# Kernel optimization log

Measured on AMD Instinct MI355X. Metric: run time of the kernel, lower is better.

## Reference

```python
import jax, jax.numpy as jnp
import numpy as np

HIDDEN = 128
STATE = 256
SEQ = 4096
BATCH = 16


def _op(q_i, q_j):
    # Binary operator for the parallel scan of the 2x2 block-diagonal recurrence.
    # m: (..., 4, N) holding [A, B, C, D] blocks; f: (..., 2, N) holding [b1, b2].
    m_i, f_i = q_i
    m_j, f_j = q_j
    iA, iB, iC, iD = m_i[..., 0, :], m_i[..., 1, :], m_i[..., 2, :], m_i[..., 3, :]
    jA, jB, jC, jD = m_j[..., 0, :], m_j[..., 1, :], m_j[..., 2, :], m_j[..., 3, :]
    m_new = jnp.stack([
        jA * iA + jB * iC,
        jA * iB + jB * iD,
        jC * iA + jD * iC,
        jC * iB + jD * iD,
    ], axis=-2)
    b1, b2 = f_i[..., 0, :], f_i[..., 1, :]
    f_new = jnp.stack([jA * b1 + jB * b2, jC * b1 + jD * b2], axis=-2) + f_j
    return m_new, f_new


def _apply_linoss_im(A_diag, B, x, step):
    # x: (L, H); B: (N, H); A_diag, step: (N,)
    Bu = x @ B.T                                    # (L, N)
    s2A = step ** 2 * A_diag
    schur = 1.0 / (1.0 + s2A)
    M11 = 1.0 - s2A * schur
    M12 = -step * A_diag * schur
    M21 = step * schur
    M22 = schur
    L, N = x.shape[0], A_diag.shape[0]
    M = jnp.broadcast_to(jnp.stack([M11, M12, M21, M22]), (L, 4, N))  # (L, 4, N)
    F = jnp.stack([M11 * Bu * step, M21 * Bu * step], axis=1)          # (L, 2, N)
    _, xs = jax.lax.associative_scan(_op, (M, F))
    return xs[:, 1, :]  # second state component y_k, shape (L, N)


def setup_inputs() -> dict:
    key = jax.random.key(0)
    kx, kA, ks, kB, kC, kD = jax.random.split(key, 6)
    x = jax.random.normal(kx, (BATCH, SEQ, HIDDEN), dtype=jnp.float32)
    A_diag = jax.random.uniform(kA, (STATE,), dtype=jnp.float32)
    steps = 0.5 * jax.random.normal(ks, (STATE,), dtype=jnp.float32)
    B = jax.random.normal(kB, (STATE, HIDDEN), dtype=jnp.float32) / np.sqrt(HIDDEN)
    C = jax.random.normal(kC, (HIDDEN, STATE), dtype=jnp.float32) / np.sqrt(STATE)
    D = jax.random.normal(kD, (HIDDEN,), dtype=jnp.float32)
    return {"x": x, "A_diag": A_diag, "steps": steps, "B": B, "C": C, "D": D}


def reference(x, A_diag, steps, B, C, D):
    # Parameter projections used by the mixer (LinOSS-IM, non-damped):
    step = jax.nn.sigmoid(steps)
    A = jax.nn.relu(A_diag)

    def per_seq(xs):
        ys = _apply_linoss_im(A, B, xs, step)   # (L, N)
        return ys @ C.T + D * xs                # (L, H)

    return jax.vmap(per_seq)(x)  # (B, L, H)
```

## Files before the change

kernel.cpp:

```cpp
#include <hip/hip_runtime.h>
#include <hip/hip_bf16.h>

#define BATCHN 16
#define SEQ 4096
#define HIDDEN 128
#define STATE 256
#define MTOT (BATCHN*SEQ)
#define NCHUNK 64
#define LCHUNK 64

typedef __bf16 bf16;
typedef __bf16 bf16x4 __attribute__((ext_vector_type(4)));
typedef __bf16 bf16x8 __attribute__((ext_vector_type(8)));
typedef float f32x4 __attribute__((ext_vector_type(4)));

__global__ __launch_bounds__(256) void setup_k(const float* __restrict__ A_diag,
        const float* __restrict__ steps, const float* __restrict__ Bm,
        const float* __restrict__ Cm, bf16* __restrict__ Bbf, bf16* __restrict__ Cbf,
        float* __restrict__ prm) {
    int idx = blockIdx.x * 256 + threadIdx.x;
    if (idx < STATE * HIDDEN) {
        Bbf[idx] = (bf16)Bm[idx];
        Cbf[idx] = (bf16)Cm[idx];
    }
    if (blockIdx.x == 0) {
        int n = threadIdx.x;
        float st = 1.0f / (1.0f + expf(-steps[n]));
        float A  = fmaxf(A_diag[n], 0.0f);
        float s2A = st * st * A;
        float schur = 1.0f / (1.0f + s2A);
        float m11 = 1.0f - s2A * schur;
        float m12 = -st * A * schur;
        float m21 = st * schur;
        float m22 = schur;
        prm[0*STATE+n] = m11;
        prm[1*STATE+n] = m12;
        prm[2*STATE+n] = m21;
        prm[3*STATE+n] = m22;
        prm[4*STATE+n] = m11 * st;
        prm[5*STATE+n] = m21 * st;
    }
}

__global__ __launch_bounds__(256) void gemm_xB(const float* __restrict__ x,
        const bf16* __restrict__ Bbf, bf16* __restrict__ Bu) {
    __shared__ bf16 lds[64][136];
    const int tid = threadIdx.x;
    const int m0 = blockIdx.x * 64;
    #pragma unroll
    for (int p = 0; p < 8; ++p) {
        int flat = p * 256 + tid;
        int row = flat >> 5;
        int c4  = flat & 31;
        float4 v = *reinterpret_cast<const float4*>(&x[(size_t)(m0 + row) * HIDDEN + c4 * 4]);
        bf16x4 w = { (bf16)v.x, (bf16)v.y, (bf16)v.z, (bf16)v.w };
        *reinterpret_cast<bf16x4*>(&lds[row][c4 * 4]) = w;
    }
    __syncthreads();
    const int wid = tid >> 6, lane = tid & 63;
    const int lr = lane & 15;
    const int lk = (lane >> 4) * 8;
    const int n0 = wid * 64;
    f32x4 acc[4][4];
    #pragma unroll
    for (int i = 0; i < 4; ++i)
        #pragma unroll
        for (int j = 0; j < 4; ++j) acc[i][j] = f32x4{0.f, 0.f, 0.f, 0.f};
    #pragma unroll
    for (int ks = 0; ks < 4; ++ks) {
        int k = ks * 32 + lk;
        bf16x8 a[4], b[4];
        #pragma unroll
        for (int mf = 0; mf < 4; ++mf)
            a[mf] = *reinterpret_cast<const bf16x8*>(&lds[mf * 16 + lr][k]);
        #pragma unroll
        for (int nf = 0; nf < 4; ++nf)
            b[nf] = *reinterpret_cast<const bf16x8*>(&Bbf[(size_t)(n0 + nf * 16 + lr) * HIDDEN + k]);
        #pragma unroll
        for (int mf = 0; mf < 4; ++mf)
            #pragma unroll
            for (int nf = 0; nf < 4; ++nf)
                acc[mf][nf] = __builtin_amdgcn_mfma_f32_16x16x32_bf16(a[mf], b[nf], acc[mf][nf], 0, 0, 0);
    }
    const int mrow = (lane >> 4) * 4;
    #pragma unroll
    for (int mf = 0; mf < 4; ++mf)
        #pragma unroll
        for (int nf = 0; nf < 4; ++nf)
            #pragma unroll
            for (int r = 0; r < 4; ++r) {
                int m = m0 + mf * 16 + mrow + r;
                int n = n0 + nf * 16 + lr;
                Bu[(size_t)m * STATE + n] = (bf16)acc[mf][nf][r];
            }
}

__global__ __launch_bounds__(256) void scan_part(const bf16* __restrict__ Bu,
        const float* __restrict__ prm, float* __restrict__ cs) {
    const int n = threadIdx.x;
    const int chunk = blockIdx.x & (NCHUNK - 1);
    const int b = blockIdx.x >> 6;
    const float m11 = prm[n], m12 = prm[STATE + n], m21 = prm[2*STATE + n],
                m22 = prm[3*STATE + n], c1 = prm[4*STATE + n], c2 = prm[5*STATE + n];
    float s1 = 0.f, s2 = 0.f;
    const bf16* p = &Bu[((size_t)(b * SEQ) + chunk * LCHUNK) * STATE + n];
    #pragma unroll 8
    for (int i = 0; i < LCHUNK; ++i) {
        float bu = (float)p[(size_t)i * STATE];
        float ns1 = fmaf(m11, s1, fmaf(m12, s2, c1 * bu));
        float ns2 = fmaf(m21, s1, fmaf(m22, s2, c2 * bu));
        s1 = ns1; s2 = ns2;
    }
    size_t base = ((size_t)(b * NCHUNK + chunk) * 2) * STATE + n;
    cs[base] = s1;
    cs[base + STATE] = s2;
}

__global__ __launch_bounds__(256) void scan_comb(float* __restrict__ cs,
        const float* __restrict__ prm) {
    const int n = threadIdx.x;
    const int b = blockIdx.x;
    float p11 = prm[n], p12 = prm[STATE + n], p21 = prm[2*STATE + n], p22 = prm[3*STATE + n];
    #pragma unroll
    for (int i = 0; i < 6; ++i) {
        float q11 = p11 * p11 + p12 * p21;
        float q12 = p11 * p12 + p12 * p22;
        float q21 = p21 * p11 + p22 * p21;
        float q22 = p21 * p12 + p22 * p22;
        p11 = q11; p12 = q12; p21 = q21; p22 = q22;
    }
    float S1 = 0.f, S2 = 0.f;
    #pragma unroll 8
    for (int c = 0; c < NCHUNK; ++c) {
        size_t base = ((size_t)(b * NCHUNK + c) * 2) * STATE + n;
        float q1 = cs[base], q2 = cs[base + STATE];
        cs[base] = S1; cs[base + STATE] = S2;
        float n1 = fmaf(p11, S1, fmaf(p12, S2, q1));
        float n2 = fmaf(p21, S1, fmaf(p22, S2, q2));
        S1 = n1; S2 = n2;
    }
}

__global__ __launch_bounds__(256) void scan_final(bf16* __restrict__ Bu,
        const float* __restrict__ prm, const float* __restrict__ cs) {
    const int n = threadIdx.x;
    const int chunk = blockIdx.x & (NCHUNK - 1);
    const int b = blockIdx.x >> 6;
    const float m11 = prm[n], m12 = prm[STATE + n], m21 = prm[2*STATE + n],
                m22 = prm[3*STATE + n], c1 = prm[4*STATE + n], c2 = prm[5*STATE + n];
    size_t cbase = ((size_t)(b * NCHUNK + chunk) * 2) * STATE + n;
    float s1 = cs[cbase], s2 = cs[cbase + STATE];
    bf16* p = &Bu[((size_t)(b * SEQ) + chunk * LCHUNK) * STATE + n];
    #pragma unroll 8
    for (int i = 0; i < LCHUNK; ++i) {
        float bu = (float)p[(size_t)i * STATE];
        float ns1 = fmaf(m11, s1, fmaf(m12, s2, c1 * bu));
        float ns2 = fmaf(m21, s1, fmaf(m22, s2, c2 * bu));
        s1 = ns1; s2 = ns2;
        p[(size_t)i * STATE] = (bf16)s2;
    }
}

__global__ __launch_bounds__(256) void gemm_yC(const bf16* __restrict__ y,
        const bf16* __restrict__ Cbf, const float* __restrict__ x,
        const float* __restrict__ Dv, float* __restrict__ out) {
    __shared__ bf16 lds[64][264];
    const int tid = threadIdx.x;
    const int m0 = blockIdx.x * 64;
    #pragma unroll
    for (int p = 0; p < 8; ++p) {
        int flat = p * 256 + tid;
        int row = flat >> 5;
        int c8  = flat & 31;
        bf16x8 v = *reinterpret_cast<const bf16x8*>(&y[(size_t)(m0 + row) * STATE + c8 * 8]);
        *reinterpret_cast<bf16x8*>(&lds[row][c8 * 8]) = v;
    }
    __syncthreads();
    const int wid = tid >> 6, lane = tid & 63;
    const int lr = lane & 15;
    const int lk = (lane >> 4) * 8;
    const int h0 = wid * 32;
    f32x4 acc[4][2];
    #pragma unroll
    for (int i = 0; i < 4; ++i) {
        acc[i][0] = f32x4{0.f, 0.f, 0.f, 0.f};
        acc[i][1] = f32x4{0.f, 0.f, 0.f, 0.f};
    }
    #pragma unroll
    for (int ks = 0; ks < 8; ++ks) {
        int k = ks * 32 + lk;
        bf16x8 a[4], bb[2];
        #pragma unroll
        for (int mf = 0; mf < 4; ++mf)
            a[mf] = *reinterpret_cast<const bf16x8*>(&lds[mf * 16 + lr][k]);
        #pragma unroll
        for (int hf = 0; hf < 2; ++hf)
            bb[hf] = *reinterpret_cast<const bf16x8*>(&Cbf[(size_t)(h0 + hf * 16 + lr) * STATE + k]);
        #pragma unroll
        for (int mf = 0; mf < 4; ++mf)
            #pragma unroll
            for (int hf = 0; hf < 2; ++hf)
                acc[mf][hf] = __builtin_amdgcn_mfma_f32_16x16x32_bf16(a[mf], bb[hf], acc[mf][hf], 0, 0, 0);
    }
    const int mrow = (lane >> 4) * 4;
    #pragma unroll
    for (int mf = 0; mf < 4; ++mf)
        #pragma unroll
        for (int hf = 0; hf < 2; ++hf) {
            int h = h0 + hf * 16 + lr;
            float d = Dv[h];
            #pragma unroll
            for (int r = 0; r < 4; ++r) {
                int m = m0 + mf * 16 + mrow + r;
                out[(size_t)m * HIDDEN + h] = acc[mf][hf][r] + d * x[(size_t)m * HIDDEN + h];
            }
        }
}

extern "C" void kernel_launch(void* const* d_in, const int* in_sizes, int n_in,
                              void* d_out, int out_size, void* d_ws, size_t ws_size,
                              hipStream_t stream) {
    const float* x      = (const float*)d_in[0];
    const float* A_diag = (const float*)d_in[1];
    const float* steps  = (const float*)d_in[2];
    const float* Bm     = (const float*)d_in[3];
    const float* Cm     = (const float*)d_in[4];
    const float* Dv     = (const float*)d_in[5];
    float* out = (float*)d_out;

    char* ws = (char*)d_ws;
    const size_t BU_BYTES = (size_t)MTOT * STATE * 2;
    const size_t CS_BYTES = (size_t)BATCHN * NCHUNK * 2 * STATE * 4;
    bf16*  Bu  = (bf16*)ws;
    float* cs  = (float*)(ws + BU_BYTES);
    bf16*  Bbf = (bf16*)(ws + BU_BYTES + CS_BYTES);
    bf16*  Cbf = (bf16*)(ws + BU_BYTES + CS_BYTES + (size_t)STATE * HIDDEN * 2);
    float* prm = (float*)(ws + BU_BYTES + CS_BYTES + (size_t)STATE * HIDDEN * 4);

    hipLaunchKernelGGL(setup_k, dim3(128), dim3(256), 0, stream, A_diag, steps, Bm, Cm, Bbf, Cbf, prm);
    hipLaunchKernelGGL(gemm_xB, dim3(MTOT / 64), dim3(256), 0, stream, x, Bbf, Bu);
    hipLaunchKernelGGL(scan_part, dim3(BATCHN * NCHUNK), dim3(256), 0, stream, Bu, prm, cs);
    hipLaunchKernelGGL(scan_comb, dim3(BATCHN), dim3(256), 0, stream, cs, prm);
    hipLaunchKernelGGL(scan_final, dim3(BATCHN * NCHUNK), dim3(256), 0, stream, Bu, prm, cs);
    hipLaunchKernelGGL(gemm_yC, dim3(MTOT / 64), dim3(256), 0, stream, Bu, Cbf, x, Dv, out);
}
```

Baseline: 69.04 us.

## Fuse GEMMs with chunked scan in LDS, recomputing x@B instead of storing Bu

Replaces the five-kernel pipeline with two fused kernels. The first computes the x@B tile into LDS and runs the intra-chunk scan to emit chunk carries. The second recomputes the same tile, applies the carried-in scan and the C projection entirely in LDS, and takes the skip term from the bf16 LDS copy of x. This removes the 32 MB bf16 Bu round trips through global memory and two launches, at the cost of doing the first GEMM twice and using more LDS per block. The skip term now uses bf16-rounded x, which slightly lowers its precision.

```diff
diff --git a/kernel.cpp b/kernel.cpp
--- a/kernel.cpp
+++ b/kernel.cpp
@@ -42,11 +42,8 @@
     }
 }
 
-__global__ __launch_bounds__(256) void gemm_xB(const float* __restrict__ x,
-        const bf16* __restrict__ Bbf, bf16* __restrict__ Bu) {
-    __shared__ bf16 lds[64][136];
-    const int tid = threadIdx.x;
-    const int m0 = blockIdx.x * 64;
+__device__ __forceinline__ void stage_x(const float* __restrict__ x, int m0, int tid,
+                                        bf16 (*xl)[136]) {
     #pragma unroll
     for (int p = 0; p < 8; ++p) {
         int flat = p * 256 + tid;
@@ -54,9 +51,12 @@
         int c4  = flat & 31;
         float4 v = *reinterpret_cast<const float4*>(&x[(size_t)(m0 + row) * HIDDEN + c4 * 4]);
         bf16x4 w = { (bf16)v.x, (bf16)v.y, (bf16)v.z, (bf16)v.w };
-        *reinterpret_cast<bf16x4*>(&lds[row][c4 * 4]) = w;
-    }
-    __syncthreads();
+        *reinterpret_cast<bf16x4*>(&xl[row][c4 * 4]) = w;
+    }
+}
+
+__device__ __forceinline__ void gemm1_to_lds(const bf16 (*xl)[136],
+        const bf16* __restrict__ Bbf, int tid, bf16 (*bu)[264]) {
     const int wid = tid >> 6, lane = tid & 63;
     const int lr = lane & 15;
     const int lk = (lane >> 4) * 8;
@@ -72,7 +72,7 @@
         bf16x8 a[4], b[4];
         #pragma unroll
         for (int mf = 0; mf < 4; ++mf)
-            a[mf] = *reinterpret_cast<const bf16x8*>(&lds[mf * 16 + lr][k]);
+            a[mf] = *reinterpret_cast<const bf16x8*>(&xl[mf * 16 + lr][k]);
         #pragma unroll
         for (int nf = 0; nf < 4; ++nf)
             b[nf] = *reinterpret_cast<const bf16x8*>(&Bbf[(size_t)(n0 + nf * 16 + lr) * HIDDEN + k]);
@@ -88,29 +88,34 @@
         #pragma unroll
         for (int nf = 0; nf < 4; ++nf)
             #pragma unroll
-            for (int r = 0; r < 4; ++r) {
-                int m = m0 + mf * 16 + mrow + r;
-                int n = n0 + nf * 16 + lr;
-                Bu[(size_t)m * STATE + n] = (bf16)acc[mf][nf][r];
-            }
-}
-
-__global__ __launch_bounds__(256) void scan_part(const bf16* __restrict__ Bu,
-        const float* __restrict__ prm, float* __restrict__ cs) {
-    const int n = threadIdx.x;
-    const int chunk = blockIdx.x & (NCHUNK - 1);
-    const int b = blockIdx.x >> 6;
+            for (int r = 0; r < 4; ++r)
+                bu[mf * 16 + mrow + r][n0 + nf * 16 + lr] = (bf16)acc[mf][nf][r];
+}
+
+__global__ __launch_bounds__(256) void k1_gemm_scanA(const float* __restrict__ x,
+        const bf16* __restrict__ Bbf, const float* __restrict__ prm,
+        float* __restrict__ cs) {
+    __shared__ bf16 xl[64][136];
+    __shared__ bf16 bu[64][264];
+    const int tid = threadIdx.x;
+    const int m0 = blockIdx.x * 64;
+    stage_x(x, m0, tid, xl);
+    __syncthreads();
+    gemm1_to_lds(xl, Bbf, tid, bu);
+    __syncthreads();
+    const int n = tid;
     const float m11 = prm[n], m12 = prm[STATE + n], m21 = prm[2*STATE + n],
                 m22 = prm[3*STATE + n], c1 = prm[4*STATE + n], c2 = prm[5*STATE + n];
     float s1 = 0.f, s2 = 0.f;
-    const bf16* p = &Bu[((size_t)(b * SEQ) + chunk * LCHUNK) * STATE + n];
     #pragma unroll 8
-    for (int i = 0; i < LCHUNK; ++i) {
-        float bu = (float)p[(size_t)i * STATE];
-        float ns1 = fmaf(m11, s1, fmaf(m12, s2, c1 * bu));
-        float ns2 = fmaf(m21, s1, fmaf(m22, s2, c2 * bu));
+    for (int t = 0; t < LCHUNK; ++t) {
+        float v = (float)bu[t][n];
+        float ns1 = fmaf(m11, s1, fmaf(m12, s2, c1 * v));
+        float ns2 = fmaf(m21, s1, fmaf(m22, s2, c2 * v));
         s1 = ns1; s2 = ns2;
     }
+    const int b = m0 >> 12;
+    const int chunk = (m0 >> 6) & (NCHUNK - 1);
     size_t base = ((size_t)(b * NCHUNK + chunk) * 2) * STATE + n;
     cs[base] = s1;
     cs[base + STATE] = s2;
@@ -141,50 +146,45 @@
     }
 }
 
-__global__ __launch_bounds__(256) void scan_final(bf16* __restrict__ Bu,
-        const float* __restrict__ prm, const float* __restrict__ cs) {
-    const int n = threadIdx.x;
-    const int chunk = blockIdx.x & (NCHUNK - 1);
-    const int b = blockIdx.x >> 6;
-    const float m11 = prm[n], m12 = prm[STATE + n], m21 = prm[2*STATE + n],
-                m22 = prm[3*STATE + n], c1 = prm[4*STATE + n], c2 = prm[5*STATE + n];
-    size_t cbase = ((size_t)(b * NCHUNK + chunk) * 2) * STATE + n;
-    float s1 = cs[cbase], s2 = cs[cbase + STATE];
-    bf16* p = &Bu[((size_t)(b * SEQ) + chunk * LCHUNK) * STATE + n];
-    #pragma unroll 8
-    for (int i = 0; i < LCHUNK; ++i) {
-        float bu = (float)p[(size_t)i * STATE];
-        float ns1 = fmaf(m11, s1, fmaf(m12, s2, c1 * bu));
-        float ns2 = fmaf(m21, s1, fmaf(m22, s2, c2 * bu));
-        s1 = ns1; s2 = ns2;
-        p[(size_t)i * STATE] = (bf16)s2;
-    }
-}
-
-__global__ __launch_bounds__(256) void gemm_yC(const bf16* __restrict__ y,
-        const bf16* __restrict__ Cbf, const float* __restrict__ x,
+__global__ __launch_bounds__(256) void k2_gemm_scan_gemm(const float* __restrict__ x,
+        const bf16* __restrict__ Bbf, const bf16* __restrict__ Cbf,
+        const float* __restrict__ prm, const float* __restrict__ cs,
         const float* __restrict__ Dv, float* __restrict__ out) {
-    __shared__ bf16 lds[64][264];
+    __shared__ bf16 xl[64][136];
+    __shared__ bf16 bu[64][264];
     const int tid = threadIdx.x;
     const int m0 = blockIdx.x * 64;
-    #pragma unroll
-    for (int p = 0; p < 8; ++p) {
-        int flat = p * 256 + tid;
-        int row = flat >> 5;
-        int c8  = flat & 31;
-        bf16x8 v = *reinterpret_cast<const bf16x8*>(&y[(size_t)(m0 + row) * STATE + c8 * 8]);
-        *reinterpret_cast<bf16x8*>(&lds[row][c8 * 8]) = v;
+    stage_x(x, m0, tid, xl);
+    __syncthreads();
+    gemm1_to_lds(xl, Bbf, tid, bu);
+    __syncthreads();
+    {
+        const int n = tid;
+        const float m11 = prm[n], m12 = prm[STATE + n], m21 = prm[2*STATE + n],
+                    m22 = prm[3*STATE + n], c1 = prm[4*STATE + n], c2 = prm[5*STATE + n];
+        const int b = m0 >> 12;
+        const int chunk = (m0 >> 6) & (NCHUNK - 1);
+        size_t cbase = ((size_t)(b * NCHUNK + chunk) * 2) * STATE + n;
+        float s1 = cs[cbase], s2 = cs[cbase + STATE];
+        #pragma unroll 8
+        for (int t = 0; t < LCHUNK; ++t) {
+            float v = (float)bu[t][n];
+            float ns1 = fmaf(m11, s1, fmaf(m12, s2, c1 * v));
+            float ns2 = fmaf(m21, s1, fmaf(m22, s2, c2 * v));
+            s1 = ns1; s2 = ns2;
+            bu[t][n] = (bf16)s2;
+        }
     }
     __syncthreads();
     const int wid = tid >> 6, lane = tid & 63;
     const int lr = lane & 15;
     const int lk = (lane >> 4) * 8;
     const int h0 = wid * 32;
-    f32x4 acc[4][2];
+    f32x4 acc2[4][2];
     #pragma unroll
     for (int i = 0; i < 4; ++i) {
-        acc[i][0] = f32x4{0.f, 0.f, 0.f, 0.f};
-        acc[i][1] = f32x4{0.f, 0.f, 0.f, 0.f};
+        acc2[i][0] = f32x4{0.f, 0.f, 0.f, 0.f};
+        acc2[i][1] = f32x4{0.f, 0.f, 0.f, 0.f};
     }
     #pragma unroll
     for (int ks = 0; ks < 8; ++ks) {
@@ -192,7 +192,7 @@
         bf16x8 a[4], bb[2];
         #pragma unroll
         for (int mf = 0; mf < 4; ++mf)
-            a[mf] = *reinterpret_cast<const bf16x8*>(&lds[mf * 16 + lr][k]);
+            a[mf] = *reinterpret_cast<const bf16x8*>(&bu[mf * 16 + lr][k]);
         #pragma unroll
         for (int hf = 0; hf < 2; ++hf)
             bb[hf] = *reinterpret_cast<const bf16x8*>(&Cbf[(size_t)(h0 + hf * 16 + lr) * STATE + k]);
@@ -200,7 +200,7 @@
         for (int mf = 0; mf < 4; ++mf)
             #pragma unroll
             for (int hf = 0; hf < 2; ++hf)
-                acc[mf][hf] = __builtin_amdgcn_mfma_f32_16x16x32_bf16(a[mf], bb[hf], acc[mf][hf], 0, 0, 0);
+                acc2[mf][hf] = __builtin_amdgcn_mfma_f32_16x16x32_bf16(a[mf], bb[hf], acc2[mf][hf], 0, 0, 0);
     }
     const int mrow = (lane >> 4) * 4;
     #pragma unroll
@@ -211,8 +211,8 @@
             float d = Dv[h];
             #pragma unroll
             for (int r = 0; r < 4; ++r) {
-                int m = m0 + mf * 16 + mrow + r;
-                out[(size_t)m * HIDDEN + h] = acc[mf][hf][r] + d * x[(size_t)m * HIDDEN + h];
+                int ml = mf * 16 + mrow + r;
+                out[(size_t)(m0 + ml) * HIDDEN + h] = acc2[mf][hf][r] + d * (float)xl[ml][h];
             }
         }
 }
@@ -229,18 +229,15 @@
     float* out = (float*)d_out;
 
     char* ws = (char*)d_ws;
-    const size_t BU_BYTES = (size_t)MTOT * STATE * 2;
     const size_t CS_BYTES = (size_t)BATCHN * NCHUNK * 2 * STATE * 4;
-    bf16*  Bu  = (bf16*)ws;
-    float* cs  = (float*)(ws + BU_BYTES);
-    bf16*  Bbf = (bf16*)(ws + BU_BYTES + CS_BYTES);
-    bf16*  Cbf = (bf16*)(ws + BU_BYTES + CS_BYTES + (size_t)STATE * HIDDEN * 2);
-    float* prm = (float*)(ws + BU_BYTES + CS_BYTES + (size_t)STATE * HIDDEN * 4);
+    float* cs  = (float*)ws;
+    bf16*  Bbf = (bf16*)(ws + CS_BYTES);
+    bf16*  Cbf = (bf16*)(ws + CS_BYTES + (size_t)STATE * HIDDEN * 2);
+    float* prm = (float*)(ws + CS_BYTES + (size_t)STATE * HIDDEN * 4);
 
     hipLaunchKernelGGL(setup_k, dim3(128), dim3(256), 0, stream, A_diag, steps, Bm, Cm, Bbf, Cbf, prm);
-    hipLaunchKernelGGL(gemm_xB, dim3(MTOT / 64), dim3(256), 0, stream, x, Bbf, Bu);
-    hipLaunchKernelGGL(scan_part, dim3(BATCHN * NCHUNK), dim3(256), 0, stream, Bu, prm, cs);
+    hipLaunchKernelGGL(k1_gemm_scanA, dim3(MTOT / 64), dim3(256), 0, stream, x, Bbf, prm, cs);
     hipLaunchKernelGGL(scan_comb, dim3(BATCHN), dim3(256), 0, stream, cs, prm);
-    hipLaunchKernelGGL(scan_final, dim3(BATCHN * NCHUNK), dim3(256), 0, stream, Bu, prm, cs);
-    hipLaunchKernelGGL(gemm_yC, dim3(MTOT / 64), dim3(256), 0, stream, Bu, Cbf, x, Dv, out);
-}
+    hipLaunchKernelGGL(k2_gemm_scan_gemm, dim3(MTOT / 64), dim3(256), 0, stream,
+                       x, Bbf, Cbf, prm, cs, Dv, out);
+}
```

Measured after the change: 56.93 us. 17.5% less time.
